# Kernel optimization log

Hardware: AMD Instinct MI355X
Metric: run time of the kernel (lower is better)

## Reference

```python
import jax, jax.numpy as jnp
import numpy as np

# NF4 codebook (bitsandbytes nf4 data type, 16 levels)
NF4_TABLE = np.array([
    -1.0, -0.6961928009986877, -0.5250730514526367, -0.39491748809814453,
    -0.28444138169288635, -0.18477343022823334, -0.09105003625154495, 0.0,
    0.07958029955625534, 0.16093020141124725, 0.24611230194568634,
    0.33791524171829224, 0.44070982933044434, 0.5626170039176941,
    0.7229568362236023, 1.0], dtype=np.float32)

BLOCKSIZE = 64
SCALING = 32.0 / 16.0  # lora_alpha / r


def setup_inputs() -> dict:
    key = jax.random.key(0)
    k1, k2, k3, k4, k5 = jax.random.split(key, 5)
    tokens, in_f, out_f, r = 256, 4096, 11008, 16
    x = jax.random.normal(k1, (tokens, in_f), dtype=jnp.float32)
    q_codes = jax.random.randint(k2, (out_f, in_f), 0, 16, dtype=jnp.int32)
    absmax = jax.random.uniform(k3, (out_f, in_f // BLOCKSIZE), dtype=jnp.float32)
    lora_A = jax.random.normal(k4, (r, in_f), dtype=jnp.float32) * (1.0 / np.sqrt(in_f))
    lora_B = jax.random.normal(k5, (out_f, r), dtype=jnp.float32) * 0.02
    return {"x": x, "q_codes": q_codes, "absmax": absmax,
            "lora_A": lora_A, "lora_B": lora_B}


def reference(x, q_codes, absmax, lora_A, lora_B):
    out_f, in_f = q_codes.shape
    nf4 = jnp.asarray(NF4_TABLE, dtype=x.dtype)
    # Dequantize: codebook lookup, then per-block absmax scale.
    W = nf4[q_codes].reshape(out_f, in_f // BLOCKSIZE, BLOCKSIZE)
    W = (W * absmax[:, :, None]).reshape(out_f, in_f)  # [out_f, in_f]
    # Base 4-bit linear (no bias in bnb Linear4bit default here).
    base = x @ W.T  # [tokens, out_f]
    # LoRA path: dropout p=0 is identity in eval; scaling = alpha/r.
    lora = (x @ lora_A.T) @ lora_B.T  # [tokens, r] -> [tokens, out_f]
    return base + lora * jnp.asarray(SCALING, dtype=x.dtype)
```

## Files before the change

kernel.cpp:

```cpp
#include <hip/hip_runtime.h>
#include <hip/hip_fp16.h>

typedef unsigned int uint;
typedef unsigned short ushort;

typedef __attribute__((ext_vector_type(8))) _Float16 f16x8;
typedef __attribute__((ext_vector_type(4))) float f32x4;

#define TOK 256
#define OUTF 11008
#define INF 4096
#define BN 64
#define NT2 172

__device__ __constant__ float NF4_TBL[16] = {
    -1.0f, -0.6961928009986877f, -0.5250730514526367f, -0.39491748809814453f,
    -0.28444138169288635f, -0.18477343022823334f, -0.09105003625154495f, 0.0f,
    0.07958029955625534f, 0.16093020141124725f, 0.24611230194568634f,
    0.33791524171829224f, 0.44070982933044434f, 0.5626170039176941f,
    0.7229568362236023f, 1.0f};

__device__ __forceinline__ ushort f2h(float f) {
  return __half_as_ushort(__float2half(f));
}

__device__ __forceinline__ float nf4v(int c, int tbits) {
  return __int_as_float(__builtin_amdgcn_ds_bpermute(c << 2, tbits));
}

__device__ __forceinline__ uint2 dq4(int4 c, __half2 ax2, int tbits) {
  __half2 h0 = __floats2half2_rn(nf4v(c.x, tbits), nf4v(c.y, tbits));
  __half2 h1 = __floats2half2_rn(nf4v(c.z, tbits), nf4v(c.w, tbits));
  h0 = __hmul2(h0, ax2);
  h1 = __hmul2(h1, ax2);
  union { __half2 h[2]; uint2 u; } r;
  r.h[0] = h0; r.h[1] = h1;
  return r.u;
}

__global__ void prep_kernel(const float* __restrict__ x, uint4* __restrict__ xf4,
                            const float4* __restrict__ lB4, ushort4* __restrict__ lBh4) {
  const int stride = gridDim.x * blockDim.x;
  const int t0 = blockIdx.x * blockDim.x + threadIdx.x;
  for (int f = t0; f < TOK * INF / 8; f += stride) {
    int l = f & 63;
    int rlo = l & 15, chunk = l >> 4;
    int ms = (f >> 6) & 7;
    int mt = ms >> 1, ks2 = ms & 1;
    int m64 = (f >> 9) & 3;
    int kb = f >> 11;
    int m = m64 * 64 + mt * 16 + rlo;
    int k0 = kb * 64 + (ks2 * 4 + chunk) * 8;
    const float4* src = (const float4*)(x + (size_t)m * INF + k0);
    float4 v0 = src[0], v1 = src[1];
    union { ushort4 h[2]; uint4 u; } pk;
    pk.h[0].x = f2h(v0.x); pk.h[0].y = f2h(v0.y); pk.h[0].z = f2h(v0.z); pk.h[0].w = f2h(v0.w);
    pk.h[1].x = f2h(v1.x); pk.h[1].y = f2h(v1.y); pk.h[1].z = f2h(v1.z); pk.h[1].w = f2h(v1.w);
    xf4[f] = pk.u;
  }
  for (int i = t0; i < OUTF * 16; i += stride) {
    int n = i >> 4, jq = i & 15;
    ushort4 o = {0, 0, 0, 0};
    if (jq < 4) {
      float4 v = lB4[n * 4 + jq];
      o.x = f2h(v.x); o.y = f2h(v.y); o.z = f2h(v.z); o.w = f2h(v.w);
    }
    lBh4[i] = o;
  }
}

__global__ __launch_bounds__(1024)
void xa_kernel(const float* __restrict__ x, const float* __restrict__ lA,
               ushort* __restrict__ xa2) {
  const int m = blockIdx.x;
  const int t = threadIdx.x;
  const float4* x4 = (const float4*)(x + (size_t)m * INF);
  const float4* lA4 = (const float4*)lA;
  float4 xv = x4[t];
  float acc[16];
#pragma unroll
  for (int j = 0; j < 16; ++j) {
    float4 a = lA4[j * (INF / 4) + t];
    acc[j] = xv.x * a.x + xv.y * a.y + xv.z * a.z + xv.w * a.w;
  }
#pragma unroll
  for (int j = 0; j < 16; ++j)
#pragma unroll
    for (int s = 32; s > 0; s >>= 1) acc[j] += __shfl_xor(acc[j], s, 64);
  __shared__ float red[16][16];
  const int w = t >> 6, l = t & 63;
  if (l == 0) {
#pragma unroll
    for (int j = 0; j < 16; ++j) red[w][j] = acc[j];
  }
  __syncthreads();
  if (t < 64) {
    ushort v = 0;
    if (t < 16) {
      float s = 0.f;
#pragma unroll
      for (int w2 = 0; w2 < 16; ++w2) s += red[w2][t];
      v = f2h(2.0f * s);
    }
    xa2[m * 64 + t] = v;
  }
}

__global__ __launch_bounds__(256, 2)
void gemm_kernel(const int* __restrict__ qc, const float* __restrict__ am,
                 const ushort* __restrict__ xf, const ushort* __restrict__ lBh,
                 const ushort* __restrict__ xa2, float* __restrict__ dest32,
                 ushort* __restrict__ dest16, int nst, int fp16out) {
  const int tid = threadIdx.x;
  const int w = tid >> 6;
  const int l = tid & 63;
  const int chunk = l >> 4;
  const int rlo = l & 15;
  const int split = blockIdx.x / NT2;
  const int ntile = blockIdx.x - split * NT2;
  const int nw0 = ntile * BN + w * 16;
  const int kb0 = split * nst;
  const int nr = nw0 + rlo;

  const int tbits = __float_as_int(NF4_TBL[l & 15]);
  const int* qrow = qc + (size_t)nr * INF + chunk * 8;
  const float* arow = am + (size_t)nr * 64;

  f32x4 acc[16];
#pragma unroll
  for (int mt = 0; mt < 16; ++mt) acc[mt] = (f32x4){0.f, 0.f, 0.f, 0.f};

  auto loadC = [&](int4 (&c)[4], float& ax, int kb) {
    const int* p = qrow + kb * 64;
    c[0] = *(const int4*)(p);
    c[1] = *(const int4*)(p + 4);
    c[2] = *(const int4*)(p + 32);
    c[3] = *(const int4*)(p + 36);
    ax = arow[kb];
  };
  auto dqB = [&](const int4 (&c)[4], float ax, f16x8& b0, f16x8& b1) {
    __half2 ax2 = __float2half2_rn(ax);
    union { uint2 u2[2]; f16x8 f; } u0, u1;
    u0.u2[0] = dq4(c[0], ax2, tbits);
    u0.u2[1] = dq4(c[1], ax2, tbits);
    u1.u2[0] = dq4(c[2], ax2, tbits);
    u1.u2[1] = dq4(c[3], ax2, tbits);
    b0 = u0.f; b1 = u1.f;
  };
  auto sweep = [&](int kb, f16x8 b0, f16x8 b1) {
    __builtin_amdgcn_s_setprio(1);
#pragma unroll
    for (int mt = 0; mt < 16; ++mt) {
      const ushort* base =
          xf + (((size_t)kb * 4 + (mt >> 2)) * 8 + (mt & 3) * 2) * 512 + l * 8;
      f16x8 a0 = *(const f16x8*)(base);
      f16x8 a1 = *(const f16x8*)(base + 512);
      acc[mt] = __builtin_amdgcn_mfma_f32_16x16x32_f16(a0, b0, acc[mt], 0, 0, 0);
      acc[mt] = __builtin_amdgcn_mfma_f32_16x16x32_f16(a1, b1, acc[mt], 0, 0, 0);
    }
    __builtin_amdgcn_s_setprio(0);
  };

  int4 cA[4], cB[4];
  float axA, axB;
  loadC(cA, axA, kb0);
  if (nst > 1) loadC(cB, axB, kb0 + 1);

  for (int s = 0; s < nst; s += 2) {
    f16x8 b0, b1;
    dqB(cA, axA, b0, b1);
    if (s + 2 < nst) loadC(cA, axA, kb0 + s + 2);
    sweep(kb0 + s, b0, b1);
    if (s + 1 < nst) {
      f16x8 b2, b3;
      dqB(cB, axB, b2, b3);
      if (s + 3 < nst) loadC(cB, axB, kb0 + s + 3);
      sweep(kb0 + s + 1, b2, b3);
    }
  }

  if (split == 0) {
    f16x8 b_l = *(const f16x8*)(lBh + (size_t)nr * 64 + chunk * 8);
#pragma unroll
    for (int mt = 0; mt < 16; ++mt) {
      f16x8 a_l = *(const f16x8*)(xa2 + (size_t)(mt * 16 + rlo) * 64 + chunk * 8);
      acc[mt] = __builtin_amdgcn_mfma_f32_16x16x32_f16(a_l, b_l, acc[mt], 0, 0, 0);
    }
  }

  if (fp16out) {
    ushort* dst = dest16 + (size_t)split * TOK * OUTF + nr;
#pragma unroll
    for (int mt = 0; mt < 16; ++mt)
#pragma unroll
      for (int r = 0; r < 4; ++r)
        dst[(size_t)(mt * 16 + chunk * 4 + r) * OUTF] = f2h(acc[mt][r]);
  } else {
    float* dst = dest32 + nr;
#pragma unroll
    for (int mt = 0; mt < 16; ++mt)
#pragma unroll
      for (int r = 0; r < 4; ++r)
        dst[(size_t)(mt * 16 + chunk * 4 + r) * OUTF] = acc[mt][r];
  }
}

__global__ void reduce_kernel(const uint4* __restrict__ part, float4* __restrict__ out,
                              int ks) {
  const int QN8 = TOK * OUTF / 8;
  int i = blockIdx.x * blockDim.x + threadIdx.x;
  if (i < QN8) {
    float s0 = 0.f, s1 = 0.f, s2 = 0.f, s3 = 0.f, s4 = 0.f, s5 = 0.f, s6 = 0.f, s7 = 0.f;
    for (int sp = 0; sp < ks; ++sp) {
      uint4 v = part[(size_t)sp * QN8 + i];
      union { uint u; __half2 h; } a, b, c, d;
      a.u = v.x; b.u = v.y; c.u = v.z; d.u = v.w;
      float2 fa = __half22float2(a.h), fb = __half22float2(b.h);
      float2 fc = __half22float2(c.h), fd = __half22float2(d.h);
      s0 += fa.x; s1 += fa.y; s2 += fb.x; s3 += fb.y;
      s4 += fc.x; s5 += fc.y; s6 += fd.x; s7 += fd.y;
    }
    out[2 * i] = (float4){s0, s1, s2, s3};
    out[2 * i + 1] = (float4){s4, s5, s6, s7};
  }
}

extern "C" void kernel_launch(void* const* d_in, const int* in_sizes, int n_in,
                              void* d_out, int out_size, void* d_ws, size_t ws_size,
                              hipStream_t stream) {
  const float* x = (const float*)d_in[0];
  const int* qc = (const int*)d_in[1];
  const float* am = (const float*)d_in[2];
  const float* lA = (const float*)d_in[3];
  const float* lB = (const float*)d_in[4];
  float* out = (float*)d_out;

  const size_t off_lB = (size_t)TOK * INF * 2;
  const size_t off_xa2 = off_lB + (size_t)OUTF * 64 * 2;
  const size_t off_part = off_xa2 + (size_t)TOK * 64 * 2;
  const size_t part_bytes = (size_t)TOK * OUTF * 2;

  ushort* xf = (ushort*)d_ws;
  ushort* lBh = (ushort*)((char*)d_ws + off_lB);
  ushort* xa2 = (ushort*)((char*)d_ws + off_xa2);
  ushort* part = (ushort*)((char*)d_ws + off_part);

  int ks = 1;
  if (ws_size >= off_part + 8 * part_bytes) ks = 8;
  else if (ws_size >= off_part + 4 * part_bytes) ks = 4;
  else if (ws_size >= off_part + 2 * part_bytes) ks = 2;
  const int fp16out = (ks > 1) ? 1 : 0;

  prep_kernel<<<2048, 256, 0, stream>>>(x, (uint4*)xf, (const float4*)lB,
                                        (ushort4*)lBh);
  xa_kernel<<<TOK, 1024, 0, stream>>>(x, lA, xa2);
  gemm_kernel<<<NT2 * ks, 256, 0, stream>>>(qc, am, xf, lBh, xa2, out, part,
                                            64 / ks, fp16out);
  if (ks > 1)
    reduce_kernel<<<(TOK * OUTF / 8 + 255) / 256, 256, 0, stream>>>((const uint4*)part,
                                                                    (float4*)out, ks);
}
```

Before: 336.3 us.

## Retile GEMM warps into 2x2 grid sharing A and B fragments

Each wave used to cover all 256 tokens for 16 output columns. It now covers 128 tokens by 32 columns, arranged as a 2x2 wave grid. Every A fragment feeds two MFMAs and every dequantized B fragment feeds eight, which halves global A loads per wave while doubling quantized-code loads and dequant work per wave. All A fragments for a k-block are also preloaded into registers before the MFMA burst, which raises register pressure and could hurt occupancy under launch_bounds(256,2).

```diff
diff --git a/kernel.cpp b/kernel.cpp
--- a/kernel.cpp
+++ b/kernel.cpp
@@ -113,95 +113,130 @@
                  ushort* __restrict__ dest16, int nst, int fp16out) {
   const int tid = threadIdx.x;
   const int w = tid >> 6;
+  const int wm = w >> 1;
+  const int wn = w & 1;
   const int l = tid & 63;
   const int chunk = l >> 4;
   const int rlo = l & 15;
   const int split = blockIdx.x / NT2;
   const int ntile = blockIdx.x - split * NT2;
-  const int nw0 = ntile * BN + w * 16;
+  const int nw0 = ntile * BN + wn * 32;
   const int kb0 = split * nst;
-  const int nr = nw0 + rlo;
 
   const int tbits = __float_as_int(NF4_TBL[l & 15]);
-  const int* qrow = qc + (size_t)nr * INF + chunk * 8;
-  const float* arow = am + (size_t)nr * 64;
-
-  f32x4 acc[16];
-#pragma unroll
-  for (int mt = 0; mt < 16; ++mt) acc[mt] = (f32x4){0.f, 0.f, 0.f, 0.f};
-
-  auto loadC = [&](int4 (&c)[4], float& ax, int kb) {
-    const int* p = qrow + kb * 64;
-    c[0] = *(const int4*)(p);
-    c[1] = *(const int4*)(p + 4);
-    c[2] = *(const int4*)(p + 32);
-    c[3] = *(const int4*)(p + 36);
-    ax = arow[kb];
-  };
-  auto dqB = [&](const int4 (&c)[4], float ax, f16x8& b0, f16x8& b1) {
-    __half2 ax2 = __float2half2_rn(ax);
-    union { uint2 u2[2]; f16x8 f; } u0, u1;
-    u0.u2[0] = dq4(c[0], ax2, tbits);
-    u0.u2[1] = dq4(c[1], ax2, tbits);
-    u1.u2[0] = dq4(c[2], ax2, tbits);
-    u1.u2[1] = dq4(c[3], ax2, tbits);
-    b0 = u0.f; b1 = u1.f;
-  };
-  auto sweep = [&](int kb, f16x8 b0, f16x8 b1) {
+  const int* qrow0 = qc + (size_t)(nw0 + rlo) * INF + chunk * 8;
+  const int* qrow1 = qc + (size_t)(nw0 + 16 + rlo) * INF + chunk * 8;
+  const float* arow0 = am + (size_t)(nw0 + rlo) * 64;
+  const float* arow1 = am + (size_t)(nw0 + 16 + rlo) * 64;
+
+  f32x4 acc[8][2];
+#pragma unroll
+  for (int mt = 0; mt < 8; ++mt)
+#pragma unroll
+    for (int nt = 0; nt < 2; ++nt) acc[mt][nt] = (f32x4){0.f, 0.f, 0.f, 0.f};
+
+  auto loadC = [&](int4 (&c)[8], float (&ax)[2], int kb) {
+    const int* p0 = qrow0 + kb * 64;
+    const int* p1 = qrow1 + kb * 64;
+    c[0] = *(const int4*)(p0);      c[1] = *(const int4*)(p0 + 4);
+    c[2] = *(const int4*)(p0 + 32); c[3] = *(const int4*)(p0 + 36);
+    c[4] = *(const int4*)(p1);      c[5] = *(const int4*)(p1 + 4);
+    c[6] = *(const int4*)(p1 + 32); c[7] = *(const int4*)(p1 + 36);
+    ax[0] = arow0[kb];
+    ax[1] = arow1[kb];
+  };
+  auto issueA = [&](f16x8 (&a)[16], int kb) {
+#pragma unroll
+    for (int mt = 0; mt < 8; ++mt)
+#pragma unroll
+      for (int ks2 = 0; ks2 < 2; ++ks2)
+        a[mt * 2 + ks2] = *(const f16x8*)(
+            xf + (((size_t)kb * 4 + wm * 2 + (mt >> 2)) * 8 + (mt & 3) * 2 + ks2) * 512 + l * 8);
+  };
+  auto dqB = [&](const int4 (&c)[8], const float (&ax)[2], f16x8 (&b)[2][2]) {
+#pragma unroll
+    for (int nt = 0; nt < 2; ++nt) {
+      __half2 ax2 = __float2half2_rn(ax[nt]);
+#pragma unroll
+      for (int ks2 = 0; ks2 < 2; ++ks2) {
+        union { uint2 u2[2]; f16x8 f; } u;
+        u.u2[0] = dq4(c[nt * 4 + ks2 * 2 + 0], ax2, tbits);
+        u.u2[1] = dq4(c[nt * 4 + ks2 * 2 + 1], ax2, tbits);
+        b[nt][ks2] = u.f;
+      }
+    }
+  };
+  auto mfma32 = [&](const f16x8 (&a)[16], const f16x8 (&b)[2][2]) {
     __builtin_amdgcn_s_setprio(1);
 #pragma unroll
-    for (int mt = 0; mt < 16; ++mt) {
-      const ushort* base =
-          xf + (((size_t)kb * 4 + (mt >> 2)) * 8 + (mt & 3) * 2) * 512 + l * 8;
-      f16x8 a0 = *(const f16x8*)(base);
-      f16x8 a1 = *(const f16x8*)(base + 512);
-      acc[mt] = __builtin_amdgcn_mfma_f32_16x16x32_f16(a0, b0, acc[mt], 0, 0, 0);
-      acc[mt] = __builtin_amdgcn_mfma_f32_16x16x32_f16(a1, b1, acc[mt], 0, 0, 0);
-    }
+    for (int ks2 = 0; ks2 < 2; ++ks2)
+#pragma unroll
+      for (int mt = 0; mt < 8; ++mt)
+#pragma unroll
+        for (int nt = 0; nt < 2; ++nt)
+          acc[mt][nt] = __builtin_amdgcn_mfma_f32_16x16x32_f16(
+              a[mt * 2 + ks2], b[nt][ks2], acc[mt][nt], 0, 0, 0);
     __builtin_amdgcn_s_setprio(0);
   };
 
-  int4 cA[4], cB[4];
-  float axA, axB;
+  int4 cA[8], cB[8];
+  float axA[2], axB[2];
+  f16x8 aF[16];
   loadC(cA, axA, kb0);
   if (nst > 1) loadC(cB, axB, kb0 + 1);
 
   for (int s = 0; s < nst; s += 2) {
-    f16x8 b0, b1;
-    dqB(cA, axA, b0, b1);
-    if (s + 2 < nst) loadC(cA, axA, kb0 + s + 2);
-    sweep(kb0 + s, b0, b1);
+    {
+      issueA(aF, kb0 + s);
+      f16x8 b[2][2];
+      dqB(cA, axA, b);
+      if (s + 2 < nst) loadC(cA, axA, kb0 + s + 2);
+      mfma32(aF, b);
+    }
     if (s + 1 < nst) {
-      f16x8 b2, b3;
-      dqB(cB, axB, b2, b3);
+      issueA(aF, kb0 + s + 1);
+      f16x8 b[2][2];
+      dqB(cB, axB, b);
       if (s + 3 < nst) loadC(cB, axB, kb0 + s + 3);
-      sweep(kb0 + s + 1, b2, b3);
+      mfma32(aF, b);
     }
   }
 
   if (split == 0) {
-    f16x8 b_l = *(const f16x8*)(lBh + (size_t)nr * 64 + chunk * 8);
-#pragma unroll
-    for (int mt = 0; mt < 16; ++mt) {
-      f16x8 a_l = *(const f16x8*)(xa2 + (size_t)(mt * 16 + rlo) * 64 + chunk * 8);
-      acc[mt] = __builtin_amdgcn_mfma_f32_16x16x32_f16(a_l, b_l, acc[mt], 0, 0, 0);
+    f16x8 b_l[2];
+    b_l[0] = *(const f16x8*)(lBh + (size_t)(nw0 + rlo) * 64 + chunk * 8);
+    b_l[1] = *(const f16x8*)(lBh + (size_t)(nw0 + 16 + rlo) * 64 + chunk * 8);
+#pragma unroll
+    for (int mt = 0; mt < 8; ++mt) {
+      f16x8 a_l = *(const f16x8*)(xa2 + (size_t)(wm * 128 + mt * 16 + rlo) * 64 + chunk * 8);
+#pragma unroll
+      for (int nt = 0; nt < 2; ++nt)
+        acc[mt][nt] = __builtin_amdgcn_mfma_f32_16x16x32_f16(a_l, b_l[nt], acc[mt][nt], 0, 0, 0);
     }
   }
 
   if (fp16out) {
-    ushort* dst = dest16 + (size_t)split * TOK * OUTF + nr;
-#pragma unroll
-    for (int mt = 0; mt < 16; ++mt)
-#pragma unroll
-      for (int r = 0; r < 4; ++r)
-        dst[(size_t)(mt * 16 + chunk * 4 + r) * OUTF] = f2h(acc[mt][r]);
+    ushort* dst = dest16 + (size_t)split * TOK * OUTF;
+#pragma unroll
+    for (int mt = 0; mt < 8; ++mt)
+#pragma unroll
+      for (int nt = 0; nt < 2; ++nt) {
+        int c = nw0 + nt * 16 + rlo;
+#pragma unroll
+        for (int r = 0; r < 4; ++r)
+          dst[(size_t)(wm * 128 + mt * 16 + chunk * 4 + r) * OUTF + c] = f2h(acc[mt][nt][r]);
+      }
   } else {
-    float* dst = dest32 + nr;
-#pragma unroll
-    for (int mt = 0; mt < 16; ++mt)
-#pragma unroll
-      for (int r = 0; r < 4; ++r)
-        dst[(size_t)(mt * 16 + chunk * 4 + r) * OUTF] = acc[mt][r];
+    float* dst = dest32;
+#pragma unroll
+    for (int mt = 0; mt < 8; ++mt)
+#pragma unroll
+      for (int nt = 0; nt < 2; ++nt) {
+        int c = nw0 + nt * 16 + rlo;
+#pragma unroll
+        for (int r = 0; r < 4; ++r)
+          dst[(size_t)(wm * 128 + mt * 16 + chunk * 4 + r) * OUTF + c] = acc[mt][nt][r];
+      }
   }
 }
 
```

Measured after the change: 335.9 us. Within noise of the previous version (-0.1%).
